# Performance work log

Measured on AMD Instinct MI355X. Metric: run time of the kernel, lower is better.

## Reference

```python
import jax, jax.numpy as jnp
import numpy as np

COMMITMENT_COST = 0.25


def setup_inputs() -> dict:
    key = jax.random.key(0)
    k1, k2 = jax.random.split(key)
    n_embeddings, embedding_dim = 1024, 256
    x = jax.random.normal(k1, (32, 2048, embedding_dim), dtype=jnp.float32)
    r = 1.0 / n_embeddings
    embedding = jax.random.uniform(k2, (n_embeddings, embedding_dim),
                                   dtype=jnp.float32, minval=-r, maxval=r)
    return {"x": x, "embedding": embedding}


def reference(x, embedding):
    M, D = embedding.shape
    # x is detached before flattening in the original quantize()
    x_flat = jax.lax.stop_gradient(x).reshape(-1, D)  # [N, D]
    distances = (jnp.sum(embedding * embedding, axis=1)
                 + jnp.sum(x_flat * x_flat, axis=1, keepdims=True)
                 - 2.0 * (x_flat @ embedding.T))  # [N, M]
    indices = jnp.argmin(distances, axis=-1)  # [N] int
    quantized = embedding[indices].reshape(x.shape)  # gather + view_as(x)
    # commitment loss: quantized is detached in the loss term
    e_latent_loss = jnp.mean(jnp.square(x - jax.lax.stop_gradient(quantized)))
    loss = COMMITMENT_COST * e_latent_loss
    return quantized, loss, indices
```

## Files before the change

kernel.cpp:

```cpp
#include <hip/hip_runtime.h>

#define N_ROWS   65536
#define D        256
#define D4       64
#define M        1024
#define LOSS_OFF 16777216
#define IDX_OFF  16777217
#define COMMIT_SCALE (0.25f / 16777216.0f)
#define E_SCALE  1024.0f
#define C_SCALE  0.001953125f

typedef _Float16 f16x8 __attribute__((ext_vector_type(8)));
typedef _Float16 f16x4 __attribute__((ext_vector_type(4)));
typedef float    f32x4 __attribute__((ext_vector_type(4)));

__device__ __forceinline__ void async_copy16(const void* g, void* l) {
    __builtin_amdgcn_global_load_lds(
        (const __attribute__((address_space(1))) unsigned int*)g,
        (__attribute__((address_space(3))) unsigned int*)l, 16, 0, 0);
}

__device__ __forceinline__ float np_block128(const float* __restrict__ a, int l) {
    float r0 = __fmul_rn(a[l +   0], a[l +   0]);
    float r1 = __fmul_rn(a[l +  16], a[l +  16]);
    float r2 = __fmul_rn(a[l +  32], a[l +  32]);
    float r3 = __fmul_rn(a[l +  48], a[l +  48]);
    float r4 = __fmul_rn(a[l +  64], a[l +  64]);
    float r5 = __fmul_rn(a[l +  80], a[l +  80]);
    float r6 = __fmul_rn(a[l +  96], a[l +  96]);
    float r7 = __fmul_rn(a[l + 112], a[l + 112]);
    return __fadd_rn(__fadd_rn(__fadd_rn(r0, r1), __fadd_rn(r2, r3)),
                     __fadd_rn(__fadd_rn(r4, r5), __fadd_rn(r6, r7)));
}
__device__ __forceinline__ float np_reduce16(float v) {
    float s = __fadd_rn(v, __shfl_down(v, 8));
    s = __fadd_rn(s, __shfl_down(s, 4));
    s = __fadd_rn(s, __shfl_down(s, 2));
    s = __fadd_rn(s, __shfl_down(s, 1));
    return s;
}

__global__ __launch_bounds__(256) void norms_kernel(
    const float4* __restrict__ x4, const float4* __restrict__ emb4,
    float* __restrict__ bsq, float* __restrict__ esq,
    _Float16* __restrict__ e_hi, _Float16* __restrict__ e_mid,
    float* __restrict__ loss_slot) {
    __shared__ float rowbuf[16 * 260];
    const int tid = threadIdx.x;
    const float4* src4;
    float* dst;
    int row0;
    const bool is_emb = blockIdx.x >= 4096;
    if (!is_emb) {
        row0 = blockIdx.x * 16;
        src4 = x4 + (size_t)row0 * 64;
        dst = bsq + row0;
    } else {
        row0 = (blockIdx.x - 4096) * 16;
        src4 = emb4 + (size_t)row0 * 64;
        dst = esq + row0;
    }
    #pragma unroll
    for (int p = 0; p < 4; ++p) {
        const int f = tid + p * 256;
        const int r = f >> 6, c4 = f & 63;
        *(float4*)&rowbuf[r * 260 + c4 * 4] = src4[f];
    }
    __syncthreads();
    const int l = tid & 15, g = tid >> 4;
    const float* base = &rowbuf[g * 260];
    const float v0 = np_block128(base, l);
    const float v1 = np_block128(base + 128, l);
    const float t0 = np_reduce16(v0);
    const float t1 = np_reduce16(v1);
    if (l == 0) dst[g] = __fadd_rn(t0, t1);
    if (blockIdx.x == 0 && tid == 0) *loss_slot = 0.0f;

    if (is_emb) {
        #pragma unroll
        for (int p = 0; p < 4; ++p) {
            const int f = tid + p * 256;
            const int r = f >> 6, k4 = f & 63;
            const int code = row0 + r;
            const int kc = k4 >> 3, k8 = k4 & 7;
            const int q = k8 >> 1, half = k8 & 1;
            const int jt = code >> 7, cl = code & 127;
            const int cg = cl >> 4, lmc = cl & 15;
            float4 v = *(const float4*)&rowbuf[r * 260 + k4 * 4];
            float a[4] = {v.x * E_SCALE, v.y * E_SCALE,
                          v.z * E_SCALE, v.w * E_SCALE};
            f16x4 hi, mid;
            #pragma unroll
            for (int j = 0; j < 4; ++j) {
                _Float16 h = (_Float16)a[j];
                float rr = __fsub_rn(a[j], (float)h);
                hi[j] = h;
                mid[j] = (_Float16)rr;
            }
            const size_t ofs = (size_t)kc * 32768 + (size_t)jt * 4096
                             + (size_t)(cg * 64 + q * 16 + lmc) * 8 + half * 4;
            *(f16x4*)&e_hi[ofs]  = hi;
            *(f16x4*)&e_mid[ofs] = mid;
        }
    }
}

__global__ __launch_bounds__(256, 2) void argmin_mfma_kernel(
    const float* __restrict__ x,
    const _Float16* __restrict__ e_hi, const _Float16* __restrict__ e_mid,
    const float* __restrict__ esq, const float* __restrict__ bsq,
    float* __restrict__ idx_out_f, int* __restrict__ idx_out_i) {
    __shared__ __attribute__((aligned(16))) _Float16 buf[2][16384];
    __shared__ float esq_lds[1024];
    __shared__ float red_d[64][2];
    __shared__ int   red_i[64][2];

    const int tid = threadIdx.x;
    const int w = tid >> 6, lane = tid & 63;
    const int w_row = w >> 1, w_col = w & 1;
    const int lm = lane & 15, q = lane >> 4;
    const int row0 = blockIdx.x * 64;

    const int p_sub = w >> 1, p_plane = w & 1;
    const _Float16* p_src = p_plane ? e_mid : e_hi;
    auto dma_group = [&](int g, int s) {
        const int jt = g >> 2, kc0 = (g & 3) * 2;
        const char* gp = (const char*)p_src
                       + (size_t)(kc0 + p_sub) * 65536 + (size_t)jt * 8192
                       + (size_t)lane * 16;
        _Float16* lp = &buf[s][p_sub * 8192 + p_plane * 4096];
        #pragma unroll
        for (int u = 0; u < 8; ++u)
            async_copy16(gp + u * 1024, lp + u * 512);
    };

    dma_group(0, 0);

    f16x8 a_hi[2][8], a_mid[2][8];
    #pragma unroll
    for (int fm = 0; fm < 2; ++fm) {
        const float* xr = x + (size_t)(row0 + w_row * 32 + fm * 16 + lm) * D + q * 8;
        #pragma unroll
        for (int kc = 0; kc < 8; ++kc) {
            float4 v0 = *(const float4*)(xr + kc * 32);
            float4 v1 = *(const float4*)(xr + kc * 32 + 4);
            float e[8] = {v0.x, v0.y, v0.z, v0.w, v1.x, v1.y, v1.z, v1.w};
            #pragma unroll
            for (int j = 0; j < 8; ++j) {
                _Float16 h = (_Float16)e[j];
                float r = __fsub_rn(e[j], (float)h);
                a_hi[fm][kc][j]  = h;
                a_mid[fm][kc][j] = (_Float16)r;
            }
        }
    }
    float bq[2][4];
    #pragma unroll
    for (int fm = 0; fm < 2; ++fm)
        #pragma unroll
        for (int r = 0; r < 4; ++r)
            bq[fm][r] = bsq[row0 + w_row * 32 + fm * 16 + q * 4 + r];

    *(float4*)&esq_lds[tid * 4] = ((const float4*)esq)[tid];

    asm volatile("s_waitcnt vmcnt(0) lgkmcnt(0)" ::: "memory");
    __syncthreads();

    float best[2][4] = {{3.0e38f, 3.0e38f, 3.0e38f, 3.0e38f},
                        {3.0e38f, 3.0e38f, 3.0e38f, 3.0e38f}};
    int bidx[2][4] = {{0, 0, 0, 0}, {0, 0, 0, 0}};

    for (int jt = 0; jt < 8; ++jt) {
        const int j0 = jt * 128;
        f32x4 acc[2][4] = {};
        #pragma unroll
        for (int gi = 0; gi < 4; ++gi) {
            const int g = jt * 4 + gi;
            if (g) {
                asm volatile("s_waitcnt vmcnt(0) lgkmcnt(0)\n\t"
                             "s_barrier" ::: "memory");
            }
            if (g < 31) dma_group(g + 1, (g + 1) & 1);
            const int s = g & 1;
            #pragma unroll
            for (int sub = 0; sub < 2; ++sub) {
                const int kc = gi * 2 + sub;
                f16x8 bh[4], bm[4];
                const int fb = sub * 8192 + (w_col * 4) * 512 + lane * 8;
                #pragma unroll
                for (int fn = 0; fn < 4; ++fn) {
                    bh[fn] = *(const f16x8*)&buf[s][fb + fn * 512];
                    bm[fn] = *(const f16x8*)&buf[s][fb + 4096 + fn * 512];
                }
                #pragma unroll
                for (int fm = 0; fm < 2; ++fm)
                    #pragma unroll
                    for (int fn = 0; fn < 4; ++fn) {
                        acc[fm][fn] = __builtin_amdgcn_mfma_f32_16x16x32_f16(
                            a_hi[fm][kc], bh[fn], acc[fm][fn], 0, 0, 0);
                        acc[fm][fn] = __builtin_amdgcn_mfma_f32_16x16x32_f16(
                            a_mid[fm][kc], bh[fn], acc[fm][fn], 0, 0, 0);
                        acc[fm][fn] = __builtin_amdgcn_mfma_f32_16x16x32_f16(
                            a_hi[fm][kc], bm[fn], acc[fm][fn], 0, 0, 0);
                    }
            }
        }
        #pragma unroll
        for (int fn = 0; fn < 4; ++fn) {
            const int j = j0 + w_col * 64 + fn * 16 + lm;
            const float eq = esq_lds[j];
            #pragma unroll
            for (int fm = 0; fm < 2; ++fm)
                #pragma unroll
                for (int r = 0; r < 4; ++r) {
                    const float d = __fsub_rn(__fadd_rn(eq, bq[fm][r]),
                                              acc[fm][fn][r] * C_SCALE);
                    if (d < best[fm][r]) { best[fm][r] = d; bidx[fm][r] = j; }
                }
        }
    }
    #pragma unroll
    for (int fm = 0; fm < 2; ++fm)
        #pragma unroll
        for (int r = 0; r < 4; ++r) {
            float d = best[fm][r]; int i = bidx[fm][r];
            #pragma unroll
            for (int mv = 1; mv <= 8; mv <<= 1) {
                const float d2 = __shfl_xor(d, mv, 64);
                const int   i2 = __shfl_xor(i, mv, 64);
                if (d2 < d || (d2 == d && i2 < i)) { d = d2; i = i2; }
            }
            best[fm][r] = d; bidx[fm][r] = i;
        }
    __syncthreads();
    if (lm == 0) {
        #pragma unroll
        for (int fm = 0; fm < 2; ++fm)
            #pragma unroll
            for (int r = 0; r < 4; ++r) {
                const int rl = w_row * 32 + fm * 16 + q * 4 + r;
                red_d[rl][w_col] = best[fm][r];
                red_i[rl][w_col] = bidx[fm][r];
            }
    }
    __syncthreads();
    if (tid < 64) {
        float d0 = red_d[tid][0]; int i0 = red_i[tid][0];
        const float d1 = red_d[tid][1]; const int i1 = red_i[tid][1];
        if (d1 < d0 || (d1 == d0 && i1 < i0)) { d0 = d1; i0 = i1; }
        idx_out_f[row0 + tid] = (float)i0;
        idx_out_i[row0 + tid] = i0;
    }
}

__global__ __launch_bounds__(256) void gather_loss_kernel(
    const float4* __restrict__ x4, const float4* __restrict__ emb4,
    const int* __restrict__ idx, float4* __restrict__ q4,
    float* __restrict__ loss_slot) {
    const int base = blockIdx.x * 256 + threadIdx.x;
    float acc = 0.0f;
    #pragma unroll
    for (int i = 0; i < 16; ++i) {
        const int f   = base + i * (1024 * 256);
        const int row = f >> 6;
        const int c4  = f & 63;
        const int e   = idx[row];
        float4 qv = emb4[e * D4 + c4];
        float4 xv = x4[f];
        q4[f] = qv;
        const float dx = xv.x - qv.x, dy = xv.y - qv.y;
        const float dz = xv.z - qv.z, dw = xv.w - qv.w;
        acc += dx * dx + dy * dy + dz * dz + dw * dw;
    }
    #pragma unroll
    for (int off = 32; off; off >>= 1) acc += __shfl_down(acc, off, 64);
    __shared__ float wsum[4];
    const int lane = threadIdx.x & 63, w = threadIdx.x >> 6;
    if (lane == 0) wsum[w] = acc;
    __syncthreads();
    if (threadIdx.x == 0) {
        atomicAdd(loss_slot, (wsum[0] + wsum[1] + wsum[2] + wsum[3]) * COMMIT_SCALE);
    }
}

extern "C" void kernel_launch(void* const* d_in, const int* in_sizes, int n_in,
                              void* d_out, int out_size, void* d_ws, size_t ws_size,
                              hipStream_t stream) {
    const float* x   = (const float*)d_in[0];
    const float* emb = (const float*)d_in[1];
    float* out = (float*)d_out;
    float*    bsq  = (float*)d_ws;
    float*    esq  = bsq + N_ROWS;
    int*      idx  = (int*)(esq + M);
    _Float16* e_hi = (_Float16*)(idx + N_ROWS);
    _Float16* e_mid = e_hi + (size_t)M * D;

    norms_kernel<<<4096 + M / 16, 256, 0, stream>>>((const float4*)x,
                                                    (const float4*)emb,
                                                    bsq, esq, e_hi, e_mid,
                                                    out + LOSS_OFF);
    argmin_mfma_kernel<<<N_ROWS / 64, 256, 0, stream>>>(x, e_hi, e_mid,
                                                        esq, bsq,
                                                        out + IDX_OFF, idx);
    gather_loss_kernel<<<1024, 256, 0, stream>>>((const float4*)x,
                                                 (const float4*)emb, idx,
                                                 (float4*)out, out + LOSS_OFF);
}
```

Before: 234.5 us.

## Fuse row norms and gather/loss into the argmin kernel

The x row-norm computation moves from the preprocessing kernel into the main argmin kernel. It stages each block's 64 rows through the second LDS buffer, and the result lives in LDS instead of global workspace. The gather of quantized rows and the commitment-loss reduction also move into the tail of the argmin kernel, which reads indices from LDS. This removes a pass over x in the norms kernel, the index round trip, and one kernel launch. In exchange the main kernel reads x up to three times (norms, fp16 split, loss), adds extra barriers before the MFMA loop, and uses more LDS, which could limit occupancy.

New measurement: 225.1 us. 1.04x faster.

```diff
diff --git a/kernel.cpp b/kernel.cpp
--- a/kernel.cpp
+++ b/kernel.cpp
@@ -40,26 +40,14 @@
     return s;
 }
 
-__global__ __launch_bounds__(256) void norms_kernel(
-    const float4* __restrict__ x4, const float4* __restrict__ emb4,
-    float* __restrict__ bsq, float* __restrict__ esq,
+__global__ __launch_bounds__(256) void emb_kernel(
+    const float4* __restrict__ emb4, float* __restrict__ esq,
     _Float16* __restrict__ e_hi, _Float16* __restrict__ e_mid,
     float* __restrict__ loss_slot) {
     __shared__ float rowbuf[16 * 260];
     const int tid = threadIdx.x;
-    const float4* src4;
-    float* dst;
-    int row0;
-    const bool is_emb = blockIdx.x >= 4096;
-    if (!is_emb) {
-        row0 = blockIdx.x * 16;
-        src4 = x4 + (size_t)row0 * 64;
-        dst = bsq + row0;
-    } else {
-        row0 = (blockIdx.x - 4096) * 16;
-        src4 = emb4 + (size_t)row0 * 64;
-        dst = esq + row0;
-    }
+    const int row0 = blockIdx.x * 16;
+    const float4* src4 = emb4 + (size_t)row0 * 64;
     #pragma unroll
     for (int p = 0; p < 4; ++p) {
         const int f = tid + p * 256;
@@ -73,53 +61,56 @@
     const float v1 = np_block128(base + 128, l);
     const float t0 = np_reduce16(v0);
     const float t1 = np_reduce16(v1);
-    if (l == 0) dst[g] = __fadd_rn(t0, t1);
+    if (l == 0) esq[row0 + g] = __fadd_rn(t0, t1);
     if (blockIdx.x == 0 && tid == 0) *loss_slot = 0.0f;
 
-    if (is_emb) {
-        #pragma unroll
-        for (int p = 0; p < 4; ++p) {
-            const int f = tid + p * 256;
-            const int r = f >> 6, k4 = f & 63;
-            const int code = row0 + r;
-            const int kc = k4 >> 3, k8 = k4 & 7;
-            const int q = k8 >> 1, half = k8 & 1;
-            const int jt = code >> 7, cl = code & 127;
-            const int cg = cl >> 4, lmc = cl & 15;
-            float4 v = *(const float4*)&rowbuf[r * 260 + k4 * 4];
-            float a[4] = {v.x * E_SCALE, v.y * E_SCALE,
-                          v.z * E_SCALE, v.w * E_SCALE};
-            f16x4 hi, mid;
-            #pragma unroll
-            for (int j = 0; j < 4; ++j) {
-                _Float16 h = (_Float16)a[j];
-                float rr = __fsub_rn(a[j], (float)h);
-                hi[j] = h;
-                mid[j] = (_Float16)rr;
-            }
-            const size_t ofs = (size_t)kc * 32768 + (size_t)jt * 4096
-                             + (size_t)(cg * 64 + q * 16 + lmc) * 8 + half * 4;
-            *(f16x4*)&e_hi[ofs]  = hi;
-            *(f16x4*)&e_mid[ofs] = mid;
-        }
-    }
-}
-
-__global__ __launch_bounds__(256, 2) void argmin_mfma_kernel(
+    #pragma unroll
+    for (int p = 0; p < 4; ++p) {
+        const int f = tid + p * 256;
+        const int r = f >> 6, k4 = f & 63;
+        const int code = row0 + r;
+        const int kc = k4 >> 3, k8 = k4 & 7;
+        const int q = k8 >> 1, half = k8 & 1;
+        const int jt = code >> 7, cl = code & 127;
+        const int cg = cl >> 4, lmc = cl & 15;
+        float4 v = *(const float4*)&rowbuf[r * 260 + k4 * 4];
+        float a[4] = {v.x * E_SCALE, v.y * E_SCALE,
+                      v.z * E_SCALE, v.w * E_SCALE};
+        f16x4 hi, mid;
+        #pragma unroll
+        for (int j = 0; j < 4; ++j) {
+            _Float16 h = (_Float16)a[j];
+            float rr = __fsub_rn(a[j], (float)h);
+            hi[j] = h;
+            mid[j] = (_Float16)rr;
+        }
+        const size_t ofs = (size_t)kc * 32768 + (size_t)jt * 4096
+                         + (size_t)(cg * 64 + q * 16 + lmc) * 8 + half * 4;
+        *(f16x4*)&e_hi[ofs]  = hi;
+        *(f16x4*)&e_mid[ofs] = mid;
+    }
+}
+
+__global__ __launch_bounds__(256, 2) void vq_kernel(
     const float* __restrict__ x,
     const _Float16* __restrict__ e_hi, const _Float16* __restrict__ e_mid,
-    const float* __restrict__ esq, const float* __restrict__ bsq,
-    float* __restrict__ idx_out_f, int* __restrict__ idx_out_i) {
+    const float* __restrict__ esq, const float4* __restrict__ emb4,
+    float4* __restrict__ q4, float* __restrict__ idx_out_f,
+    float* __restrict__ loss_slot) {
     __shared__ __attribute__((aligned(16))) _Float16 buf[2][16384];
     __shared__ float esq_lds[1024];
+    __shared__ float bsq_lds[64];
+    __shared__ int   idx_lds[64];
     __shared__ float red_d[64][2];
     __shared__ int   red_i[64][2];
+    __shared__ float wsum[4];
 
     const int tid = threadIdx.x;
     const int w = tid >> 6, lane = tid & 63;
     const int w_row = w >> 1, w_col = w & 1;
     const int lm = lane & 15, q = lane >> 4;
     const int row0 = blockIdx.x * 64;
+    const float4* x4 = (const float4*)x;
 
     const int p_sub = w >> 1, p_plane = w & 1;
     const _Float16* p_src = p_plane ? e_mid : e_hi;
@@ -136,6 +127,29 @@
 
     dma_group(0, 0);
 
+    {
+        float* rowstage = (float*)&buf[1][0];
+        const int l = tid & 15, g16 = tid >> 4;
+        #pragma unroll 1
+        for (int rr = 0; rr < 4; ++rr) {
+            const float4* src4 = x4 + (size_t)(row0 + rr * 16) * 64;
+            #pragma unroll
+            for (int p = 0; p < 4; ++p) {
+                const int f = tid + p * 256;
+                const int r = f >> 6, c4 = f & 63;
+                *(float4*)&rowstage[r * 260 + c4 * 4] = src4[f];
+            }
+            __syncthreads();
+            const float* base = &rowstage[g16 * 260];
+            const float v0 = np_block128(base, l);
+            const float v1 = np_block128(base + 128, l);
+            const float t0 = np_reduce16(v0);
+            const float t1 = np_reduce16(v1);
+            if (l == 0) bsq_lds[rr * 16 + g16] = __fadd_rn(t0, t1);
+            __syncthreads();
+        }
+    }
+
     f16x8 a_hi[2][8], a_mid[2][8];
     #pragma unroll
     for (int fm = 0; fm < 2; ++fm) {
@@ -159,7 +173,7 @@
     for (int fm = 0; fm < 2; ++fm)
         #pragma unroll
         for (int r = 0; r < 4; ++r)
-            bq[fm][r] = bsq[row0 + w_row * 32 + fm * 16 + q * 4 + r];
+            bq[fm][r] = bsq_lds[w_row * 32 + fm * 16 + q * 4 + r];
 
     *(float4*)&esq_lds[tid * 4] = ((const float4*)esq)[tid];
 
@@ -249,38 +263,31 @@
         const float d1 = red_d[tid][1]; const int i1 = red_i[tid][1];
         if (d1 < d0 || (d1 == d0 && i1 < i0)) { d0 = d1; i0 = i1; }
         idx_out_f[row0 + tid] = (float)i0;
-        idx_out_i[row0 + tid] = i0;
-    }
-}
-
-__global__ __launch_bounds__(256) void gather_loss_kernel(
-    const float4* __restrict__ x4, const float4* __restrict__ emb4,
-    const int* __restrict__ idx, float4* __restrict__ q4,
-    float* __restrict__ loss_slot) {
-    const int base = blockIdx.x * 256 + threadIdx.x;
-    float acc = 0.0f;
-    #pragma unroll
-    for (int i = 0; i < 16; ++i) {
-        const int f   = base + i * (1024 * 256);
-        const int row = f >> 6;
-        const int c4  = f & 63;
-        const int e   = idx[row];
+        idx_lds[tid] = i0;
+    }
+    __syncthreads();
+
+    float accl = 0.0f;
+    #pragma unroll
+    for (int k = 0; k < 16; ++k) {
+        const int f = tid + k * 256;
+        const int row = f >> 6, c4 = f & 63;
+        const int e = idx_lds[row];
+        const size_t gofs = (size_t)(row0 + row) * 64 + c4;
         float4 qv = emb4[e * D4 + c4];
-        float4 xv = x4[f];
-        q4[f] = qv;
+        float4 xv = x4[gofs];
+        q4[gofs] = qv;
         const float dx = xv.x - qv.x, dy = xv.y - qv.y;
         const float dz = xv.z - qv.z, dw = xv.w - qv.w;
-        acc += dx * dx + dy * dy + dz * dz + dw * dw;
-    }
-    #pragma unroll
-    for (int off = 32; off; off >>= 1) acc += __shfl_down(acc, off, 64);
-    __shared__ float wsum[4];
-    const int lane = threadIdx.x & 63, w = threadIdx.x >> 6;
-    if (lane == 0) wsum[w] = acc;
-    __syncthreads();
-    if (threadIdx.x == 0) {
-        atomicAdd(loss_slot, (wsum[0] + wsum[1] + wsum[2] + wsum[3]) * COMMIT_SCALE);
-    }
+        accl += dx * dx + dy * dy + dz * dz + dw * dw;
+    }
+    #pragma unroll
+    for (int off = 32; off; off >>= 1) accl += __shfl_down(accl, off, 64);
+    if (lane == 0) wsum[w] = accl;
+    __syncthreads();
+    if (tid == 0)
+        atomicAdd(loss_slot,
+                  (wsum[0] + wsum[1] + wsum[2] + wsum[3]) * COMMIT_SCALE);
 }
 
 extern "C" void kernel_launch(void* const* d_in, const int* in_sizes, int n_in,
@@ -289,20 +296,14 @@
     const float* x   = (const float*)d_in[0];
     const float* emb = (const float*)d_in[1];
     float* out = (float*)d_out;
-    float*    bsq  = (float*)d_ws;
-    float*    esq  = bsq + N_ROWS;
-    int*      idx  = (int*)(esq + M);
-    _Float16* e_hi = (_Float16*)(idx + N_ROWS);
+    float*    esq  = (float*)d_ws;
+    _Float16* e_hi = (_Float16*)(esq + M);
     _Float16* e_mid = e_hi + (size_t)M * D;
 
-    norms_kernel<<<4096 + M / 16, 256, 0, stream>>>((const float4*)x,
-                                                    (const float4*)emb,
-                                                    bsq, esq, e_hi, e_mid,
-                                                    out + LOSS_OFF);
-    argmin_mfma_kernel<<<N_ROWS / 64, 256, 0, stream>>>(x, e_hi, e_mid,
-                                                        esq, bsq,
-                                                        out + IDX_OFF, idx);
-    gather_loss_kernel<<<1024, 256, 0, stream>>>((const float4*)x,
-                                                 (const float4*)emb, idx,
-                                                 (float4*)out, out + LOSS_OFF);
-}
+    emb_kernel<<<M / 16, 256, 0, stream>>>((const float4*)emb, esq,
+                                           e_hi, e_mid, out + LOSS_OFF);
+    vq_kernel<<<N_ROWS / 64, 256, 0, stream>>>(x, e_hi, e_mid, esq,
+                                               (const float4*)emb,
+                                               (float4*)out, out + IDX_OFF,
+                                               out + LOSS_OFF);
+}
```
